# Optimization experiments

Measured on AMD Instinct MI355X. Metric: run time of the kernel, lower is better.

## Reference

```python
import jax, jax.numpy as jnp
import numpy as np

C = 256
CR = 32  # C // nc_reduce

def setup_inputs() -> dict:
    key = jax.random.key(0)
    ks = jax.random.split(key, 8)
    B, H, W = 4, 64, 64
    x = jax.random.normal(ks[0], (B, C, H, W), dtype=jnp.float32)
    s_in = 1.0 / np.sqrt(C)
    Wq = jax.random.uniform(ks[1], (CR, C), jnp.float32, -s_in, s_in)
    bq = jax.random.uniform(ks[2], (CR,), jnp.float32, -s_in, s_in)
    Wk = jax.random.uniform(ks[3], (CR, C), jnp.float32, -s_in, s_in)
    bk = jax.random.uniform(ks[4], (CR,), jnp.float32, -s_in, s_in)
    Wv = jax.random.uniform(ks[5], (C, C), jnp.float32, -s_in, s_in)
    bv = jax.random.uniform(ks[6], (C,), jnp.float32, -s_in, s_in)
    gamma = jnp.zeros((1,), dtype=jnp.float32)
    return {"x": x, "Wq": Wq, "bq": bq, "Wk": Wk, "bk": bk,
            "Wv": Wv, "bv": bv, "gamma": gamma}

def reference(x, Wq, bq, Wk, bk, Wv, bv, gamma):
    B, Cc, H, W = x.shape
    N = H * W
    xf = x.reshape(B, Cc, N)                       # [B, C, N]
    # 1x1 convs == per-position channel projections
    q = jnp.einsum('dc,bcn->bdn', Wq, xf) + bq[None, :, None]  # [B, CR, N]
    k = jnp.einsum('dc,bcn->bdn', Wk, xf) + bk[None, :, None]  # [B, CR, N]
    v = jnp.einsum('dc,bcn->bdn', Wv, xf) + bv[None, :, None]  # [B, C, N]
    # energy[b,i,j] = q[:, :, i] . k[:, :, j]  (no scaling, as in source)
    energy = jnp.einsum('bdi,bdj->bij', q, k)      # [B, N, N]
    attn = jax.nn.softmax(energy, axis=-1)
    # out[b,c,i] = sum_j v[b,c,j] * attn[b,i,j]
    outv = jnp.einsum('bcj,bij->bci', v, attn)     # [B, C, N]
    out = gamma[0] * outv.reshape(B, Cc, H, W) + x
    return out
```

## Files before the change

### kernel.cpp

```cpp
#include <hip/hip_runtime.h>
#include <hip/hip_bf16.h>

#define NB 4
#define CCH 256
#define CRD 32
#define NN 4096

typedef __attribute__((ext_vector_type(8))) short short8;
typedef __attribute__((ext_vector_type(4))) float floatx4;
typedef __attribute__((ext_vector_type(4))) int intx4;
typedef __attribute__((ext_vector_type(2))) unsigned int uintx2;

__device__ __forceinline__ unsigned short f2bf(float f) {
  unsigned u = __builtin_bit_cast(unsigned, f);
  u += 0x7FFFu + ((u >> 16) & 1u);
  return (unsigned short)(u >> 16);
}

__device__ __forceinline__ unsigned short f2bf_c(float f) {
  f = fminf(fmaxf(f, -1.0e4f), 1.0e4f);
  unsigned u = __builtin_bit_cast(unsigned, f);
  u += 0x7FFFu + ((u >> 16) & 1u);
  return (unsigned short)(u >> 16);
}

__device__ __forceinline__ unsigned pack2c(float a, float b) {
  return (unsigned)f2bf_c(a) | ((unsigned)f2bf_c(b) << 16);
}

__device__ __forceinline__ float sat(float v) {
  return fminf(fmaxf(v, -1.0e30f), 1.0e30f);
}

__device__ __forceinline__ short8 ld_frag_g(const unsigned short* p) {
  return __builtin_bit_cast(short8, *(const intx4*)p);
}

__global__ __launch_bounds__(256) void w_convert(
    const float* __restrict__ Wq, const float* __restrict__ Wk,
    const float* __restrict__ Wv, unsigned short* __restrict__ Wb)
{
  const int t    = blockIdx.x * 256 + threadIdx.x;
  const int row  = t >> 6;
  const int col4 = t & 63;
  const float* src = (row < 32) ? Wq + (size_t)row * CCH
                   : (row < 64) ? Wk + (size_t)(row - 32) * CCH
                                : Wv + (size_t)(row - 64) * CCH;
  const floatx4 f = *(const floatx4*)(src + col4 * 4);
  uintx2 u;
  u[0] = pack2c(f[0], f[1]);
  u[1] = pack2c(f[2], f[3]);
  *(uintx2*)(Wb + (size_t)row * CCH + col4 * 4) = u;
}

__global__ __launch_bounds__(256) void gemm_qkv_fused(
    const float* __restrict__ x, const unsigned short* __restrict__ Wb,
    const float* __restrict__ bq, const float* __restrict__ bk,
    const float* __restrict__ bv,
    unsigned short* __restrict__ qT, unsigned short* __restrict__ kT,
    unsigned short* __restrict__ vv)
{
  __shared__ __align__(16) unsigned short xs[64 * 264];
  __shared__ __align__(16) unsigned short ws[64 * 264];

  const int tid  = threadIdx.x;
  const int wave = tid >> 6;
  const int lane = tid & 63;
  const int lq   = lane >> 4;
  const int lm   = lane & 15;
  const int n0   = blockIdx.x << 6;
  const int mg   = blockIdx.y;
  const int b    = blockIdx.z;

  {
    const int nn = lane;
    const int cg = wave;
    const float* xb = x + ((size_t)b << 20) + n0 + nn;
#pragma unroll
    for (int it = 0; it < 16; ++it) {
      const int c0 = it * 16 + cg * 4;
      const float v0 = xb[(size_t)(c0 + 0) << 12];
      const float v1 = xb[(size_t)(c0 + 1) << 12];
      const float v2 = xb[(size_t)(c0 + 2) << 12];
      const float v3 = xb[(size_t)(c0 + 3) << 12];
      uintx2 u;
      u[0] = pack2c(v0, v1);
      u[1] = pack2c(v2, v3);
      *(uintx2*)(xs + nn * 264 + c0) = u;
    }
  }

  const int mt_lo = mg ? 3 : 0;
  const int mt_hi = mg ? 5 : 3;

  for (int mt = mt_lo; mt < mt_hi; ++mt) {
#pragma unroll
    for (int i = 0; i < 8; ++i) {
      const int u = i * 256 + tid;
      const int m = u >> 5;
      const int o = (u & 31) * 8;
      *(intx4*)(ws + m * 264 + o) =
          *(const intx4*)(Wb + (size_t)(mt * 64 + m) * CCH + o);
    }
    __syncthreads();

    floatx4 acc[4];
#pragma unroll
    for (int t = 0; t < 4; ++t) acc[t] = (floatx4){0.f, 0.f, 0.f, 0.f};

#pragma unroll
    for (int k0 = 0; k0 < 8; ++k0) {
      short8 af[4];
#pragma unroll
      for (int ms = 0; ms < 4; ++ms)
        af[ms] = __builtin_bit_cast(short8,
            *(const intx4*)(ws + (ms * 16 + lm) * 264 + k0 * 32 + lq * 8));
      const short8 bf = __builtin_bit_cast(short8,
          *(const intx4*)(xs + (wave * 16 + lm) * 264 + k0 * 32 + lq * 8));
#pragma unroll
      for (int ms = 0; ms < 4; ++ms)
        acc[ms] = __builtin_amdgcn_mfma_f32_16x16x32_bf16(af[ms], bf,
                                                          acc[ms], 0, 0, 0);
    }
    __syncthreads();

    if (mt == 0) {
      const int n = n0 + wave * 16 + lm;
#pragma unroll
      for (int ms = 0; ms < 4; ++ms) {
        const int d0 = (ms & 1) * 16 + lq * 4;
        const float* bias = (ms < 2) ? bq : bk;
        unsigned short* dst = (ms < 2) ? qT : kT;
        uintx2 u;
        u[0] = pack2c(acc[ms][0] + bias[d0],     acc[ms][1] + bias[d0 + 1]);
        u[1] = pack2c(acc[ms][2] + bias[d0 + 2], acc[ms][3] + bias[d0 + 3]);
        *(uintx2*)(dst + (size_t)(b * NN + n) * CRD + d0) = u;
      }
    } else {
      const int cb = (mt - 1) * 64;
      unsigned short* vb2 = ws;
#pragma unroll
      for (int ms = 0; ms < 4; ++ms)
#pragma unroll
        for (int r = 0; r < 4; ++r) {
          const int c = ms * 16 + lq * 4 + r;
          vb2[c * 64 + wave * 16 + lm] = f2bf_c(acc[ms][r] + bv[cb + c]);
        }
      __syncthreads();
#pragma unroll
      for (int it = 0; it < 2; ++it) {
        const int u = it * 256 + tid;
        const int m = u >> 3;
        const int o = (u & 7) * 8;
        *(intx4*)(vv + (size_t)(b * CCH + cb + m) * NN + n0 + o) =
            *(const intx4*)(vb2 + m * 64 + o);
      }
      __syncthreads();
    }
  }
}

__global__ __launch_bounds__(512) void attn_kernel(
    const float* __restrict__ x, const float* __restrict__ gamma_p,
    const unsigned short* __restrict__ qT, const unsigned short* __restrict__ kT,
    const unsigned short* __restrict__ vv, float* __restrict__ out)
{
  __shared__ __align__(16) unsigned char smem[65536 + 2 * 2 * 4352];

  const int tid  = threadIdx.x;
  const int wave = tid >> 6;
  const int wg   = wave >> 2;
  const int cs   = wave & 3;
  const int lane = tid & 63;
  const int lq   = lane >> 4;
  const int lm   = lane & 15;
  const int xcd = blockIdx.x & 7;
  const int pos = blockIdx.x >> 3;
  const int b   = xcd >> 1;
  const int i0  = (((xcd & 1) << 5) | pos) << 6;

  const unsigned short* kTb = kT + (size_t)b * NN * CRD;
  const unsigned short* vb  = vv + (size_t)b * CCH * NN;

  short8 qf[2];
#pragma unroll
  for (int f = 0; f < 2; ++f)
    qf[f] = ld_frag_g(qT +
        (size_t)(b * NN + i0 + wg * 32 + f * 16 + lm) * CRD + lq * 8);

  int vs_g[4];
  int vs_off[4];
#pragma unroll
  for (int m = 0; m < 4; ++m) {
    const int u  = m * 512 + tid;
    const int c  = u >> 3;
    const int jb = u & 7;
    vs_g[m]   = c * NN + jb * 8;
    vs_off[m] = c * 128 + ((jb ^ (c & 7)) * 16);
  }

  floatx4 acc[8];
#pragma unroll
  for (int t = 0; t < 8; ++t) acc[t] = (floatx4){0.f, 0.f, 0.f, 0.f};
  float lsum[8] = {0.f, 0.f, 0.f, 0.f, 0.f, 0.f, 0.f, 0.f};

  intx4 vreg[4];
#pragma unroll
  for (int m = 0; m < 4; ++m)
    vreg[m] = *(const intx4*)(vb + vs_g[m]);
  short8 kf = ld_frag_g(kTb + (size_t)(cs * 16 + lm) * CRD + lq * 8);

  const floatx4 zf = {0.f, 0.f, 0.f, 0.f};

#pragma unroll 1
  for (int k = 0; k < 64; ++k) {
    unsigned char* vbuf = smem + ((k & 1) << 15);
    unsigned char* pb   = smem + 65536 + (k & 1) * 8704 + wg * 4352;

#pragma unroll
    for (int m = 0; m < 4; ++m)
      *(intx4*)(vbuf + vs_off[m]) = vreg[m];

#pragma unroll
    for (int f = 0; f < 2; ++f) {
      floatx4 S = __builtin_amdgcn_mfma_f32_16x16x32_bf16(qf[f], kf, zf, 0, 0, 0);
#pragma unroll
      for (int r = 0; r < 4; ++r) {
        const float p = __expf(fminf(fmaxf(S[r], -40.f), 40.f));
        lsum[f * 4 + r] += p;
        *(unsigned short*)(pb + (f * 16 + lq * 4 + r) * 136 +
                           ((cs * 16 + lm) << 1)) = f2bf(p);
      }
    }

    __syncthreads();

    if (k < 63) {
      const int j0n = (k + 1) << 6;
#pragma unroll
      for (int m = 0; m < 4; ++m)
        vreg[m] = *(const intx4*)(vb + vs_g[m] + j0n);
      kf = ld_frag_g(kTb + (size_t)(j0n + cs * 16 + lm) * CRD + lq * 8);
    }

#pragma unroll
    for (int ks = 0; ks < 2; ++ks) {
      short8 pf[2];
#pragma unroll
      for (int f = 0; f < 2; ++f) {
        const unsigned char* pa = pb + (f * 16 + lm) * 136 + ks * 64 + lq * 16;
        struct U128 { unsigned long long a, b; } pp;
        pp.a = *(const unsigned long long*)pa;
        pp.b = *(const unsigned long long*)(pa + 8);
        pf[f] = __builtin_bit_cast(short8, pp);
      }
#pragma unroll
      for (int nt = 0; nt < 4; ++nt) {
        const int c = cs * 64 + nt * 16 + lm;
        const short8 vf = __builtin_bit_cast(
            short8,
            *(const intx4*)(vbuf + c * 128 + (((ks * 4 + lq) ^ (lm & 7)) * 16)));
#pragma unroll
        for (int f = 0; f < 2; ++f)
          acc[f * 4 + nt] = __builtin_amdgcn_mfma_f32_16x16x32_bf16(
              pf[f], vf, acc[f * 4 + nt], 0, 0, 0);
      }
    }
  }

#pragma unroll
  for (int e = 0; e < 8; ++e) {
    float v = lsum[e];
    v += __shfl_xor(v, 1);
    v += __shfl_xor(v, 2);
    v += __shfl_xor(v, 4);
    v += __shfl_xor(v, 8);
    lsum[e] = v;
  }
  __syncthreads();
  float* lbuf = (float*)smem;
  {
    const int base = (wave * 64 + lane) * 8;
#pragma unroll
    for (int e = 0; e < 8; ++e) lbuf[base + e] = lsum[e];
  }
  __syncthreads();
  float inv[8];
#pragma unroll
  for (int e = 0; e < 8; ++e) {
    float v = 0.f;
#pragma unroll
    for (int q = 0; q < 4; ++q)
      v += lbuf[((wg * 4 + q) * 64 + lane) * 8 + e];
    inv[e] = 1.0f / v;
  }

  const float gm = gamma_p[0];
#pragma unroll
  for (int f = 0; f < 2; ++f)
#pragma unroll
    for (int nt = 0; nt < 4; ++nt) {
      const int c = cs * 64 + nt * 16 + lm;
      const int i = i0 + wg * 32 + f * 16 + lq * 4;
      const size_t idx = (size_t)(b * CCH + c) * NN + i;
      const floatx4 xv = *(const floatx4*)(x + idx);
      floatx4 o;
#pragma unroll
      for (int r = 0; r < 4; ++r)
        o[r] = gm * sat(acc[f * 4 + nt][r] * inv[f * 4 + r]) + xv[r];
      *(floatx4*)(out + idx) = o;
    }
}

extern "C" void kernel_launch(void* const* d_in, const int* in_sizes, int n_in,
                              void* d_out, int out_size, void* d_ws, size_t ws_size,
                              hipStream_t stream) {
  (void)in_sizes; (void)n_in; (void)out_size; (void)ws_size;
  const float* x     = (const float*)d_in[0];
  const float* Wq    = (const float*)d_in[1];
  const float* bq    = (const float*)d_in[2];
  const float* Wk    = (const float*)d_in[3];
  const float* bk    = (const float*)d_in[4];
  const float* Wv    = (const float*)d_in[5];
  const float* bv    = (const float*)d_in[6];
  const float* gamma = (const float*)d_in[7];

  unsigned short* qT = (unsigned short*)d_ws;
  unsigned short* kT = qT + (size_t)NB * NN * CRD;
  unsigned short* vv = kT + (size_t)NB * NN * CRD;
  unsigned short* Wb = (unsigned short*)d_out;

  w_convert<<<dim3(80), 256, 0, stream>>>(Wq, Wk, Wv, Wb);
  gemm_qkv_fused<<<dim3(64, 2, 4), 256, 0, stream>>>(x, Wb, bq, bk, bv,
                                                     qT, kT, vv);
  attn_kernel<<<dim3(256, 1, 1), 512, 0, stream>>>(x, gamma, qT, kT, vv,
                                                   (float*)d_out);
}
```

Before: 162.6 us.

## Fuse weight conversion into QKV GEMM and halve attention block query tile

Removes the separate weight-conversion kernel and instead converts fp32 weights to bf16 while loading them into shared memory inside the QKV GEMM, saving a launch and a global round trip. The attention kernel now uses 256-thread blocks, each covering 32 query rows instead of 64, launched as 512 blocks to fill more compute units. This means each block reloads the full V and K stream for half as many queries, doubling V traffic from L2. An s_setprio raise around the PV MFMA section is added to favour the matrix work.

```diff
diff --git a/kernel.cpp b/kernel.cpp
--- a/kernel.cpp
+++ b/kernel.cpp
@@ -36,27 +36,11 @@
   return __builtin_bit_cast(short8, *(const intx4*)p);
 }
 
-__global__ __launch_bounds__(256) void w_convert(
-    const float* __restrict__ Wq, const float* __restrict__ Wk,
-    const float* __restrict__ Wv, unsigned short* __restrict__ Wb)
-{
-  const int t    = blockIdx.x * 256 + threadIdx.x;
-  const int row  = t >> 6;
-  const int col4 = t & 63;
-  const float* src = (row < 32) ? Wq + (size_t)row * CCH
-                   : (row < 64) ? Wk + (size_t)(row - 32) * CCH
-                                : Wv + (size_t)(row - 64) * CCH;
-  const floatx4 f = *(const floatx4*)(src + col4 * 4);
-  uintx2 u;
-  u[0] = pack2c(f[0], f[1]);
-  u[1] = pack2c(f[2], f[3]);
-  *(uintx2*)(Wb + (size_t)row * CCH + col4 * 4) = u;
-}
-
 __global__ __launch_bounds__(256) void gemm_qkv_fused(
-    const float* __restrict__ x, const unsigned short* __restrict__ Wb,
-    const float* __restrict__ bq, const float* __restrict__ bk,
-    const float* __restrict__ bv,
+    const float* __restrict__ x,
+    const float* __restrict__ Wq, const float* __restrict__ bq,
+    const float* __restrict__ Wk, const float* __restrict__ bk,
+    const float* __restrict__ Wv, const float* __restrict__ bv,
     unsigned short* __restrict__ qT, unsigned short* __restrict__ kT,
     unsigned short* __restrict__ vv)
 {
@@ -95,12 +79,18 @@
 
   for (int mt = mt_lo; mt < mt_hi; ++mt) {
 #pragma unroll
-    for (int i = 0; i < 8; ++i) {
-      const int u = i * 256 + tid;
-      const int m = u >> 5;
-      const int o = (u & 31) * 8;
-      *(intx4*)(ws + m * 264 + o) =
-          *(const intx4*)(Wb + (size_t)(mt * 64 + m) * CCH + o);
+    for (int i = 0; i < 16; ++i) {
+      const int u  = i * 256 + tid;
+      const int m  = u >> 6;
+      const int o4 = (u & 63) * 4;
+      const float* src = (mt == 0)
+          ? (m < 32 ? Wq + (size_t)m * CCH : Wk + (size_t)(m - 32) * CCH)
+          : Wv + (size_t)((mt - 1) * 64 + m) * CCH;
+      const floatx4 f = *(const floatx4*)(src + o4);
+      uintx2 uu;
+      uu[0] = pack2c(f[0], f[1]);
+      uu[1] = pack2c(f[2], f[3]);
+      *(uintx2*)(ws + m * 264 + o4) = uu;
     }
     __syncthreads();
 
@@ -160,24 +150,22 @@
   }
 }
 
-__global__ __launch_bounds__(512) void attn_kernel(
+__global__ __launch_bounds__(256) void attn_kernel(
     const float* __restrict__ x, const float* __restrict__ gamma_p,
     const unsigned short* __restrict__ qT, const unsigned short* __restrict__ kT,
     const unsigned short* __restrict__ vv, float* __restrict__ out)
 {
-  __shared__ __align__(16) unsigned char smem[65536 + 2 * 2 * 4352];
+  __shared__ __align__(16) unsigned char smem[65536 + 2 * 4352];
 
   const int tid  = threadIdx.x;
-  const int wave = tid >> 6;
-  const int wg   = wave >> 2;
-  const int cs   = wave & 3;
+  const int cs   = tid >> 6;
   const int lane = tid & 63;
   const int lq   = lane >> 4;
   const int lm   = lane & 15;
   const int xcd = blockIdx.x & 7;
-  const int pos = blockIdx.x >> 3;
+  const int p   = blockIdx.x >> 3;
   const int b   = xcd >> 1;
-  const int i0  = (((xcd & 1) << 5) | pos) << 6;
+  const int i0  = (((xcd & 1) << 6) | p) << 5;
 
   const unsigned short* kTb = kT + (size_t)b * NN * CRD;
   const unsigned short* vb  = vv + (size_t)b * CCH * NN;
@@ -185,14 +173,13 @@
   short8 qf[2];
 #pragma unroll
   for (int f = 0; f < 2; ++f)
-    qf[f] = ld_frag_g(qT +
-        (size_t)(b * NN + i0 + wg * 32 + f * 16 + lm) * CRD + lq * 8);
-
-  int vs_g[4];
-  int vs_off[4];
-#pragma unroll
-  for (int m = 0; m < 4; ++m) {
-    const int u  = m * 512 + tid;
+    qf[f] = ld_frag_g(qT + (size_t)(b * NN + i0 + f * 16 + lm) * CRD + lq * 8);
+
+  int vs_g[8];
+  int vs_off[8];
+#pragma unroll
+  for (int m = 0; m < 8; ++m) {
+    const int u  = m * 256 + tid;
     const int c  = u >> 3;
     const int jb = u & 7;
     vs_g[m]   = c * NN + jb * 8;
@@ -204,9 +191,9 @@
   for (int t = 0; t < 8; ++t) acc[t] = (floatx4){0.f, 0.f, 0.f, 0.f};
   float lsum[8] = {0.f, 0.f, 0.f, 0.f, 0.f, 0.f, 0.f, 0.f};
 
-  intx4 vreg[4];
-#pragma unroll
-  for (int m = 0; m < 4; ++m)
+  intx4 vreg[8];
+#pragma unroll
+  for (int m = 0; m < 8; ++m)
     vreg[m] = *(const intx4*)(vb + vs_g[m]);
   short8 kf = ld_frag_g(kTb + (size_t)(cs * 16 + lm) * CRD + lq * 8);
 
@@ -215,10 +202,10 @@
 #pragma unroll 1
   for (int k = 0; k < 64; ++k) {
     unsigned char* vbuf = smem + ((k & 1) << 15);
-    unsigned char* pb   = smem + 65536 + (k & 1) * 8704 + wg * 4352;
-
-#pragma unroll
-    for (int m = 0; m < 4; ++m)
+    unsigned char* pb   = smem + 65536 + (k & 1) * 4352;
+
+#pragma unroll
+    for (int m = 0; m < 8; ++m)
       *(intx4*)(vbuf + vs_off[m]) = vreg[m];
 
 #pragma unroll
@@ -226,10 +213,10 @@
       floatx4 S = __builtin_amdgcn_mfma_f32_16x16x32_bf16(qf[f], kf, zf, 0, 0, 0);
 #pragma unroll
       for (int r = 0; r < 4; ++r) {
-        const float p = __expf(fminf(fmaxf(S[r], -40.f), 40.f));
-        lsum[f * 4 + r] += p;
+        const float pv = __expf(fminf(fmaxf(S[r], -40.f), 40.f));
+        lsum[f * 4 + r] += pv;
         *(unsigned short*)(pb + (f * 16 + lq * 4 + r) * 136 +
-                           ((cs * 16 + lm) << 1)) = f2bf(p);
+                           ((cs * 16 + lm) << 1)) = f2bf(pv);
       }
     }
 
@@ -238,11 +225,12 @@
     if (k < 63) {
       const int j0n = (k + 1) << 6;
 #pragma unroll
-      for (int m = 0; m < 4; ++m)
+      for (int m = 0; m < 8; ++m)
         vreg[m] = *(const intx4*)(vb + vs_g[m] + j0n);
       kf = ld_frag_g(kTb + (size_t)(j0n + cs * 16 + lm) * CRD + lq * 8);
     }
 
+    __builtin_amdgcn_s_setprio(1);
 #pragma unroll
     for (int ks = 0; ks < 2; ++ks) {
       short8 pf[2];
@@ -266,6 +254,7 @@
               pf[f], vf, acc[f * 4 + nt], 0, 0, 0);
       }
     }
+    __builtin_amdgcn_s_setprio(0);
   }
 
 #pragma unroll
@@ -280,7 +269,7 @@
   __syncthreads();
   float* lbuf = (float*)smem;
   {
-    const int base = (wave * 64 + lane) * 8;
+    const int base = (cs * 64 + lane) * 8;
 #pragma unroll
     for (int e = 0; e < 8; ++e) lbuf[base + e] = lsum[e];
   }
@@ -291,7 +280,7 @@
     float v = 0.f;
 #pragma unroll
     for (int q = 0; q < 4; ++q)
-      v += lbuf[((wg * 4 + q) * 64 + lane) * 8 + e];
+      v += lbuf[(q * 64 + lane) * 8 + e];
     inv[e] = 1.0f / v;
   }
 
@@ -301,7 +290,7 @@
 #pragma unroll
     for (int nt = 0; nt < 4; ++nt) {
       const int c = cs * 64 + nt * 16 + lm;
-      const int i = i0 + wg * 32 + f * 16 + lq * 4;
+      const int i = i0 + f * 16 + lq * 4;
       const size_t idx = (size_t)(b * CCH + c) * NN + i;
       const floatx4 xv = *(const floatx4*)(x + idx);
       floatx4 o;
@@ -328,11 +317,9 @@
   unsigned short* qT = (unsigned short*)d_ws;
   unsigned short* kT = qT + (size_t)NB * NN * CRD;
   unsigned short* vv = kT + (size_t)NB * NN * CRD;
-  unsigned short* Wb = (unsigned short*)d_out;
-
-  w_convert<<<dim3(80), 256, 0, stream>>>(Wq, Wk, Wv, Wb);
-  gemm_qkv_fused<<<dim3(64, 2, 4), 256, 0, stream>>>(x, Wb, bq, bk, bv,
+
+  gemm_qkv_fused<<<dim3(64, 2, 4), 256, 0, stream>>>(x, Wq, bq, Wk, bk, Wv, bv,
                                                      qT, kT, vv);
-  attn_kernel<<<dim3(256, 1, 1), 512, 0, stream>>>(x, gamma, qT, kT, vv,
+  attn_kernel<<<dim3(512, 1, 1), 256, 0, stream>>>(x, gamma, qT, kT, vv,
                                                    (float*)d_out);
 }
```

Measured after the change: 169.7 us. +4.4%, slower.
